# Kernel tuning notes

Measured on AMD Instinct MI355X. Metric: run time of the kernel, lower is better.

## Reference

```python
import jax, jax.numpy as jnp
import numpy as np

K = 9            # kernel_size * dilation
ALPHA = 0.2      # LeakyReLU slope in GAT attention
LRELU = 0.01     # Grapher.layer1 default LeakyReLU slope
EPS_NORM = 1e-12
BN_EPS = 1e-5
NEG_INF = -9e15


def setup_inputs() -> dict:
    key = jax.random.key(0)
    ks = jax.random.split(key, 9)
    B, C, H, W = 16, 64, 32, 32
    nheads, nhid = 4, 15
    return {
        "x": jax.random.normal(ks[0], (B, C, H, W), jnp.float32),
        "W_heads": jax.random.normal(ks[1], (nheads, C, nhid), jnp.float32) * 0.2,
        "a_heads": jax.random.normal(ks[2], (nheads, 2 * nhid, 1), jnp.float32) * 0.2,
        "W_out": jax.random.normal(ks[3], (nheads * nhid, C), jnp.float32) * 0.2,
        "a_out": jax.random.normal(ks[4], (2 * C, 1), jnp.float32) * 0.2,
        "conv_w": jax.random.normal(ks[5], (C, C), jnp.float32) * 0.1,
        "conv_b": jax.random.normal(ks[6], (C,), jnp.float32) * 0.1,
        "bn_gamma": jnp.ones((C,), jnp.float32),
        "bn_beta": jnp.zeros((C,), jnp.float32),
    }


def _gat_layer(h, adj, W, a, concat):
    # h: [B,N,Fin], W: [Fin,Fout], a: [2*Fout,1]
    Wh = h @ W                                   # [B,N,Fout]
    Fout = W.shape[1]
    f1 = Wh @ a[:Fout]                           # [B,N,1]  (a . Wh_i)
    f2 = Wh @ a[Fout:]                           # [B,N,1]  (a . Wh_j)
    e = jax.nn.leaky_relu(f1 + jnp.swapaxes(f2, 1, 2), ALPHA)  # [B,N,N]
    att = jnp.where(adj > 0, e, NEG_INF)
    att = jax.nn.softmax(att, axis=1)            # torch F.softmax(dim=1)
    hp = att @ Wh                                # [B,N,Fout]
    return jax.nn.elu(hp) if concat else hp


def reference(x, W_heads, a_heads, W_out, a_out, conv_w, conv_b, bn_gamma, bn_beta):
    B, C, H, W = x.shape
    N = H * W
    res = x
    xf = x.reshape(B, C, N)                      # [B,C,N]
    # F.normalize(p=2, dim=1)
    nrm = jnp.maximum(jnp.linalg.norm(xf, axis=1, keepdims=True), EPS_NORM)
    h = jnp.swapaxes(xf / nrm, 1, 2)             # [B,N,C]
    # KNN adjacency (built under no_grad in the original)
    hs = jax.lax.stop_gradient(h)
    sq = jnp.sum(hs * hs, axis=-1, keepdims=True)        # [B,N,1]
    dist = sq - 2.0 * (hs @ jnp.swapaxes(hs, 1, 2)) + jnp.swapaxes(sq, 1, 2)
    _, idx = jax.lax.top_k(-dist, K)                      # [B,N,K]
    adj = jnp.zeros((B, N, N), x.dtype).at[
        jnp.arange(B)[:, None, None], jnp.arange(N)[None, :, None], idx
    ].set(1.0)
    # 4-head GAT (dropout is identity in eval mode)
    heads = [_gat_layer(h, adj, W_heads[i], a_heads[i], True)
             for i in range(W_heads.shape[0])]
    hcat = jnp.concatenate(heads, axis=2)        # [B,N,60]
    out = jax.nn.elu(_gat_layer(hcat, adj, W_out, a_out, False))  # [B,N,C]
    y = jnp.swapaxes(out, 1, 2).reshape(B, C, H, W)
    y = jax.nn.leaky_relu(y, LRELU)
    # 1x1 conv + BatchNorm (eval: running_mean=0, running_var=1)
    y = jnp.einsum('bchw,oc->bohw', y, conv_w) + conv_b[None, :, None, None]
    y = y / jnp.sqrt(1.0 + BN_EPS) * bn_gamma[None, :, None, None] + bn_beta[None, :, None, None]
    return y + res
```

## Files before the change

kernel.cpp:

```cpp
#include <hip/hip_runtime.h>
#include <math.h>

#define NB 16
#define NC 64
#define NN 1024
#define NK 9
#define NH 4
#define NF 15

#define OFF_HN     0
#define OFF_SQV    1048576
#define OFF_IDX    1064960
#define OFF_DEN1   1212416
#define OFF_U1     1277952
#define OFF_DEN2   1278976
#define OFF_U2     1295360
#define OFF_F11    1296384
#define OFF_F21    1361920
#define OFF_F12    1427456
#define OFF_F22    1443840
#define OFF_E1     1460224
#define OFF_E2     2050048
#define OFF_WH1    2197504
#define OFF_HCAT   3246080
#define OFF_WH2    4294656
#define OFF_YTIL   5343232
#define OFF_DIST   6391808
#define ZERO_BASE  OFF_DEN1
#define ZERO_LEN   83968

__device__ __forceinline__ unsigned fkey(float x){
  unsigned b = __float_as_uint(x);
  return (b & 0x80000000u) ? ~b : (b | 0x80000000u);
}
__device__ __forceinline__ float eluf(float x){ return x > 0.f ? x : expm1f(x); }

__global__ __launch_bounds__(256) void k1_norm_wh(const float* __restrict__ x,
    const float* __restrict__ W_heads, const float* __restrict__ a_heads,
    float* __restrict__ hn, float* __restrict__ sqv, float* __restrict__ Wh1,
    float* __restrict__ f1, float* __restrict__ f2, float* __restrict__ ws){
  int t = blockIdx.x*256 + threadIdx.x;
  if (t < ZERO_LEN) ws[ZERO_BASE + t] = 0.f;
  if (t >= NB*NN) return;
  int b = t >> 10, n = t & 1023;
  const float* xb = x + b*NC*NN;
  float* hb = hn + b*NC*NN;
  float s = 0.f;
  #pragma unroll
  for (int c = 0; c < NC; c++){ float v = xb[c*NN + n]; s = fmaf(v, v, s); }
  float nrm = fmaxf(sqrtf(s), 1e-12f);
  float wh[NH][NF];
  #pragma unroll
  for (int hh = 0; hh < NH; hh++)
    #pragma unroll
    for (int f = 0; f < NF; f++) wh[hh][f] = 0.f;
  float s2 = 0.f;
  for (int c = 0; c < NC; c++){
    float v = xb[c*NN + n] / nrm;
    hb[c*NN + n] = v;
    s2 = fmaf(v, v, s2);
    #pragma unroll
    for (int hh = 0; hh < NH; hh++){
      const float* W = W_heads + (hh*NC + c)*NF;
      #pragma unroll
      for (int f = 0; f < NF; f++) wh[hh][f] = fmaf(v, W[f], wh[hh][f]);
    }
  }
  sqv[t] = s2;
  float* orow = Wh1 + ((size_t)(b*NN) + n)*64;
  #pragma unroll
  for (int hh = 0; hh < NH; hh++){
    const float* al = a_heads + hh*2*NF;
    float s1 = 0.f, sb = 0.f;
    #pragma unroll
    for (int f = 0; f < NF; f++){ s1 = fmaf(wh[hh][f], al[f], s1); sb = fmaf(wh[hh][f], al[NF+f], sb); }
    float4* o4 = (float4*)(orow + hh*16);
    o4[0] = make_float4(wh[hh][0], wh[hh][1], wh[hh][2], wh[hh][3]);
    o4[1] = make_float4(wh[hh][4], wh[hh][5], wh[hh][6], wh[hh][7]);
    o4[2] = make_float4(wh[hh][8], wh[hh][9], wh[hh][10], wh[hh][11]);
    o4[3] = make_float4(wh[hh][12], wh[hh][13], wh[hh][14], 0.f);
    int hb2 = hh*NB + b;
    f1[hb2*NN + n] = s1; f2[hb2*NN + n] = sb;
  }
}

__global__ __launch_bounds__(256) void k2a_dist(const float* __restrict__ hn,
    const float* __restrict__ sqv, float* __restrict__ dist){
  __shared__ float As[64][128];
  __shared__ float Bs[64][128];
  int b = blockIdx.y;
  int i0 = (blockIdx.x >> 3) * 128, j0 = (blockIdx.x & 7) * 128;
  const float* hb = hn + b*NC*NN;
  for (int t = threadIdx.x; t < 64*128; t += 256){
    int c = t >> 7, ii = t & 127;
    As[c][ii] = hb[c*NN + i0 + ii];
    Bs[c][ii] = hb[c*NN + j0 + ii];
  }
  __syncthreads();
  int tx = threadIdx.x & 15, ty = threadIdx.x >> 4;
  float acc[8][8];
  #pragma unroll
  for (int q = 0; q < 8; q++)
    #pragma unroll
    for (int jj = 0; jj < 8; jj++) acc[q][jj] = 0.f;
  #pragma unroll 4
  for (int c = 0; c < 64; c++){
    float4 a0 = *(const float4*)&As[c][ty*8];
    float4 a1 = *(const float4*)&As[c][ty*8+4];
    float4 b0 = *(const float4*)&Bs[c][tx*8];
    float4 b1 = *(const float4*)&Bs[c][tx*8+4];
    float av[8], bv[8];
    av[0]=a0.x; av[1]=a0.y; av[2]=a0.z; av[3]=a0.w; av[4]=a1.x; av[5]=a1.y; av[6]=a1.z; av[7]=a1.w;
    bv[0]=b0.x; bv[1]=b0.y; bv[2]=b0.z; bv[3]=b0.w; bv[4]=b1.x; bv[5]=b1.y; bv[6]=b1.z; bv[7]=b1.w;
    #pragma unroll
    for (int q = 0; q < 8; q++)
      #pragma unroll
      for (int jj = 0; jj < 8; jj++) acc[q][jj] = fmaf(av[q], bv[jj], acc[q][jj]);
  }
  const float* sv = sqv + b*NN;
  float sj[8];
  #pragma unroll
  for (int jj = 0; jj < 8; jj++) sj[jj] = sv[j0 + tx*8 + jj];
  #pragma unroll
  for (int q = 0; q < 8; q++){
    float si = sv[i0 + ty*8 + q];
    float o0[8];
    #pragma unroll
    for (int jj = 0; jj < 8; jj++) o0[jj] = (si - 2.f*acc[q][jj]) + sj[jj];
    float* dp = dist + (size_t)((b*NN) + i0 + ty*8 + q)*NN + j0 + tx*8;
    *(float4*)&dp[0] = make_float4(o0[0],o0[1],o0[2],o0[3]);
    *(float4*)&dp[4] = make_float4(o0[4],o0[5],o0[6],o0[7]);
  }
}

__global__ __launch_bounds__(256) void k2b_top9e(const float* __restrict__ dist,
    int* __restrict__ idxb, const float* __restrict__ f1, const float* __restrict__ f2,
    float* __restrict__ e1, float* __restrict__ den1){
  __shared__ int sj[4][16];
  int wave = threadIdx.x >> 6, lane = threadIdx.x & 63;
  int t = blockIdx.x*4 + wave;
  int b = t >> 10, i = t & 1023;
  const float* dr = dist + (size_t)t*NN;
  unsigned long long key[16];
  #pragma unroll
  for (int m = 0; m < 16; m++){
    int j = m*64 + lane;
    key[m] = ((unsigned long long)fkey(dr[j]) << 32) | (unsigned)j;
  }
  for (int round = 0; round < NK; round++){
    unsigned long long best = key[0];
    #pragma unroll
    for (int m = 1; m < 16; m++) best = key[m] < best ? key[m] : best;
    #pragma unroll
    for (int off = 32; off >= 1; off >>= 1){
      unsigned long long o = __shfl_xor(best, off);
      best = o < best ? o : best;
    }
    if (lane == 0) sj[wave][round] = (int)(best & 0xFFFFFFFFu);
    int wl = (int)(best & 63u);
    int wm = (int)((best >> 6) & 15u);
    if (lane == wl) key[wm] = ~0ull;
  }
  __syncthreads();
  if (lane < NK) idxb[(size_t)t*NK + lane] = sj[wave][lane];
  if (lane < 36){
    int k = lane >> 2, hh = lane & 3;
    int j = sj[wave][k];
    int hb = hh*NB + b;
    float e = f1[hb*NN + i] + f2[hb*NN + j];
    e = e >= 0.f ? e : 0.2f*e;
    e1[(size_t)(hb*NN + i)*NK + k] = e;
    atomicAdd(den1 + hb*NN + j, expf(e));
  }
}

__global__ __launch_bounds__(256) void k4b_u1(const float* __restrict__ denom1,
                       const float* __restrict__ Wh1, float* __restrict__ u1){
  int t = blockIdx.x*256 + threadIdx.x;
  if (denom1[t] != 0.f) return;
  int hb = t >> 10, j = t & 1023;
  int hh = hb >> 4, b = hb & 15;
  const float* w = Wh1 + ((size_t)(b*NN) + j)*64 + hh*16;
  for (int f = 0; f < NF; f++) atomicAdd(u1 + hb*16 + f, w[f] * (1.f/1024.f));
}

__global__ __launch_bounds__(256) void k5_hp1(const int* __restrict__ idxb, const float* __restrict__ e1,
    const float* __restrict__ denom1, const float* __restrict__ Wh1,
    const float* __restrict__ u1, float* __restrict__ hcat){
  int wave = threadIdx.x >> 6, lane = threadIdx.x & 63;
  int t = blockIdx.x*4 + wave;
  int b = t >> 10, i = t & 1023;
  int hh = lane >> 4, f = lane & 15;
  int hb = hh*NB + b;
  float acc = u1[hb*16 + f];
  const int* jp = idxb + (size_t)t*NK;
  const float* ep = e1 + (size_t)(hb*NN + i)*NK;
  const float* dn = denom1 + hb*NN;
  const float* wbase = Wh1 + ((size_t)(b*NN))*64;
  #pragma unroll 3
  for (int k = 0; k < NK; k++){
    int j = jp[k];
    float att = expf(ep[k]) / dn[j];
    acc = fmaf(att, wbase[(size_t)j*64 + lane], acc);
  }
  if (f < NF) hcat[((size_t)(b*NN) + i)*64 + hh*NF + f] = eluf(acc);
}

__global__ __launch_bounds__(256) void k7_wh2(const float* __restrict__ hcat,
    const float* __restrict__ W_out, const float* __restrict__ a_out,
    float* __restrict__ Wh2, float* __restrict__ f1, float* __restrict__ f2){
  __shared__ float hcl[64][65];
  __shared__ float p1[4][64], p2[4][64];
  int b = blockIdx.y, n0 = blockIdx.x*64;
  for (int t = threadIdx.x; t < 4096; t += 256){
    int nl = t >> 6, c = t & 63;
    hcl[nl][c] = hcat[(size_t)((b*NN) + n0 + nl)*64 + c];
  }
  __syncthreads();
  int nl = threadIdx.x & 63;
  int wv = threadIdx.x >> 6;
  int og = __builtin_amdgcn_readfirstlane(wv * 16);
  float z[16];
  #pragma unroll
  for (int m = 0; m < 16; m++) z[m] = 0.f;
  for (int c = 0; c < 60; c++){
    float yv = hcl[nl][c];
    #pragma unroll
    for (int m = 0; m < 16; m++) z[m] = fmaf(yv, W_out[c*64 + og + m], z[m]);
  }
  int n = n0 + nl;
  float* o = Wh2 + ((size_t)(b*NN) + n)*64 + og;
  #pragma unroll
  for (int m = 0; m < 16; m += 4) *(float4*)&o[m] = make_float4(z[m],z[m+1],z[m+2],z[m+3]);
  float s1 = 0.f, s2 = 0.f;
  #pragma unroll
  for (int m = 0; m < 16; m++){ s1 = fmaf(z[m], a_out[og+m], s1); s2 = fmaf(z[m], a_out[64+og+m], s2); }
  p1[wv][nl] = s1; p2[wv][nl] = s2;
  __syncthreads();
  if (threadIdx.x < 64){
    f1[b*NN + n0 + threadIdx.x] = p1[0][threadIdx.x] + p1[1][threadIdx.x] + p1[2][threadIdx.x] + p1[3][threadIdx.x];
    f2[b*NN + n0 + threadIdx.x] = p2[0][threadIdx.x] + p2[1][threadIdx.x] + p2[2][threadIdx.x] + p2[3][threadIdx.x];
  }
}

__global__ __launch_bounds__(256) void k8_edge2(const int* __restrict__ idxb, const float* __restrict__ f1,
                         const float* __restrict__ f2, float* __restrict__ e2,
                         float* __restrict__ denom2){
  int t = blockIdx.x*256 + threadIdx.x;
  int bi = t / 9;
  int b = bi >> 10;
  int j = idxb[t];
  float e = f1[bi] + f2[b*NN + j];
  e = e >= 0.f ? e : 0.2f*e;
  e2[t] = e;
  atomicAdd(denom2 + b*NN + j, expf(e));
}

__global__ __launch_bounds__(256) void k8b_u2(const float* __restrict__ denom2,
                       const float* __restrict__ Wh2, float* __restrict__ u2){
  int t = blockIdx.x*256 + threadIdx.x;
  if (denom2[t] != 0.f) return;
  int b = t >> 10;
  const float* w = Wh2 + (size_t)t*64;
  for (int f = 0; f < 64; f++) atomicAdd(u2 + b*64 + f, w[f] * (1.f/1024.f));
}

__global__ __launch_bounds__(256) void k9_hp2(const int* __restrict__ idxb, const float* __restrict__ e2,
    const float* __restrict__ denom2, const float* __restrict__ Wh2,
    const float* __restrict__ u2, float* __restrict__ ytil){
  int wave = threadIdx.x >> 6, lane = threadIdx.x & 63;
  int t = blockIdx.x*4 + wave;
  int b = t >> 10;
  float acc = u2[b*64 + lane];
  const int* jp = idxb + (size_t)t*NK;
  const float* ep = e2 + (size_t)t*NK;
  const float* dn = denom2 + b*NN;
  const float* wbase = Wh2 + ((size_t)(b*NN))*64;
  #pragma unroll 3
  for (int k = 0; k < NK; k++){
    int j = jp[k];
    float att = expf(ep[k]) / dn[j];
    acc = fmaf(att, wbase[(size_t)j*64 + lane], acc);
  }
  float v = eluf(acc);
  ytil[(size_t)t*64 + lane] = v >= 0.f ? v : 0.01f*v;
}

__global__ __launch_bounds__(256) void k11_conv(const float* __restrict__ ytil,
    const float* __restrict__ conv_w, const float* __restrict__ conv_b,
    const float* __restrict__ bn_g, const float* __restrict__ bn_b,
    const float* __restrict__ x, float* __restrict__ out){
  __shared__ float yt[64][65];
  int b = blockIdx.y, n0 = blockIdx.x*64;
  for (int t = threadIdx.x; t < 4096; t += 256){
    int nl = t >> 6, c = t & 63;
    yt[nl][c] = ytil[(size_t)((b*NN) + n0 + nl)*64 + c];
  }
  __syncthreads();
  int nl = threadIdx.x & 63;
  int og = __builtin_amdgcn_readfirstlane((int)(threadIdx.x >> 6) * 16);
  float z[16];
  #pragma unroll
  for (int m = 0; m < 16; m++) z[m] = 0.f;
  for (int c = 0; c < 64; c++){
    float yv = yt[nl][c];
    #pragma unroll
    for (int m = 0; m < 16; m++) z[m] = fmaf(yv, conv_w[(og+m)*64 + c], z[m]);
  }
  const float scbn = 1.f / sqrtf(1.f + 1e-5f);
  #pragma unroll
  for (int m = 0; m < 16; m++){
    int o = og + m;
    size_t oi = ((size_t)(b*64 + o))*NN + n0 + nl;
    out[oi] = fmaf(z[m] + conv_b[o], bn_g[o]*scbn, bn_b[o]) + x[oi];
  }
}

extern "C" void kernel_launch(void* const* d_in, const int* in_sizes, int n_in,
                              void* d_out, int out_size, void* d_ws, size_t ws_size,
                              hipStream_t stream){
  (void)in_sizes; (void)n_in; (void)out_size; (void)ws_size;
  const float* x       = (const float*)d_in[0];
  const float* W_heads = (const float*)d_in[1];
  const float* a_heads = (const float*)d_in[2];
  const float* W_out   = (const float*)d_in[3];
  const float* a_out   = (const float*)d_in[4];
  const float* conv_w  = (const float*)d_in[5];
  const float* conv_b  = (const float*)d_in[6];
  const float* bn_g    = (const float*)d_in[7];
  const float* bn_b    = (const float*)d_in[8];
  float* ws  = (float*)d_ws;
  float* out = (float*)d_out;

  float* hn   = ws + OFF_HN;
  float* sqv  = ws + OFF_SQV;
  int*   idxb = (int*)(ws + OFF_IDX);
  float* den1 = ws + OFF_DEN1;
  float* u1   = ws + OFF_U1;
  float* den2 = ws + OFF_DEN2;
  float* u2   = ws + OFF_U2;
  float* f11  = ws + OFF_F11;
  float* f21  = ws + OFF_F21;
  float* f12  = ws + OFF_F12;
  float* f22  = ws + OFF_F22;
  float* e1   = ws + OFF_E1;
  float* e2   = ws + OFF_E2;
  float* Wh1  = ws + OFF_WH1;
  float* hcat = ws + OFF_HCAT;
  float* Wh2  = ws + OFF_WH2;
  float* ytil = ws + OFF_YTIL;
  float* dist = ws + OFF_DIST;

  k1_norm_wh<<<dim3(328), dim3(256), 0, stream>>>(x, W_heads, a_heads, hn, sqv, Wh1, f11, f21, ws);
  k2a_dist<<<dim3(64,16), dim3(256), 0, stream>>>(hn, sqv, dist);
  k2b_top9e<<<dim3(4096), dim3(256), 0, stream>>>(dist, idxb, f11, f21, e1, den1);
  k4b_u1<<<dim3(256), dim3(256), 0, stream>>>(den1, Wh1, u1);
  k5_hp1<<<dim3(4096), dim3(256), 0, stream>>>(idxb, e1, den1, Wh1, u1, hcat);
  k7_wh2<<<dim3(16,16), dim3(256), 0, stream>>>(hcat, W_out, a_out, Wh2, f12, f22);
  k8_edge2<<<dim3(576), dim3(256), 0, stream>>>(idxb, f12, f22, e2, den2);
  k8b_u2<<<dim3(64), dim3(256), 0, stream>>>(den2, Wh2, u2);
  k9_hp2<<<dim3(4096), dim3(256), 0, stream>>>(idxb, e2, den2, Wh2, u2, ytil);
  k11_conv<<<dim3(16,16), dim3(256), 0, stream>>>(ytil, conv_w, conv_b, bn_g, bn_b, x, out);
}
```

Baseline: 270.3 us.

## Fuse KNN distance GEMM with per-row top-9 selection and edge scoring

Replaces the separate distance-matrix kernel and top-k kernel with one kernel that tiles the Gram product over 64-column tiles in shared memory and keeps a per-thread sorted 9-entry candidate list, then merges four partial lists per row with shuffles. This removes writing and re-reading the full B×N×N distance buffer in global memory and one launch. In exchange only 256 blocks run, each thread holds many 64-bit registers for the candidate list, and the insertion step is serial and branchy, which may limit occupancy and parallelism.

```diff
diff --git a/kernel.cpp b/kernel.cpp
--- a/kernel.cpp
+++ b/kernel.cpp
@@ -25,7 +25,6 @@
 #define OFF_HCAT   3246080
 #define OFF_WH2    4294656
 #define OFF_YTIL   5343232
-#define OFF_DIST   6391808
 #define ZERO_BASE  OFF_DEN1
 #define ZERO_LEN   83968
 
@@ -84,93 +83,107 @@
   }
 }
 
-__global__ __launch_bounds__(256) void k2a_dist(const float* __restrict__ hn,
-    const float* __restrict__ sqv, float* __restrict__ dist){
-  __shared__ float As[64][128];
-  __shared__ float Bs[64][128];
-  int b = blockIdx.y;
-  int i0 = (blockIdx.x >> 3) * 128, j0 = (blockIdx.x & 7) * 128;
+#define LSTR 68
+__global__ __launch_bounds__(256) void k2_knn(const float* __restrict__ hn,
+    const float* __restrict__ sqv, const float* __restrict__ f1g, const float* __restrict__ f2g,
+    int* __restrict__ idxb, float* __restrict__ e1, float* __restrict__ den1){
+  __shared__ float As[64][LSTR];
+  __shared__ float Bs[64][LSTR];
+  __shared__ float Ds[64][LSTR];
+  __shared__ float ssq[64], sjq[64];
+  int b  = blockIdx.y;
+  int i0 = blockIdx.x * 64;
+  int tid = threadIdx.x;
   const float* hb = hn + b*NC*NN;
-  for (int t = threadIdx.x; t < 64*128; t += 256){
-    int c = t >> 7, ii = t & 127;
-    As[c][ii] = hb[c*NN + i0 + ii];
-    Bs[c][ii] = hb[c*NN + j0 + ii];
-  }
-  __syncthreads();
-  int tx = threadIdx.x & 15, ty = threadIdx.x >> 4;
-  float acc[8][8];
-  #pragma unroll
-  for (int q = 0; q < 8; q++)
-    #pragma unroll
-    for (int jj = 0; jj < 8; jj++) acc[q][jj] = 0.f;
-  #pragma unroll 4
-  for (int c = 0; c < 64; c++){
-    float4 a0 = *(const float4*)&As[c][ty*8];
-    float4 a1 = *(const float4*)&As[c][ty*8+4];
-    float4 b0 = *(const float4*)&Bs[c][tx*8];
-    float4 b1 = *(const float4*)&Bs[c][tx*8+4];
-    float av[8], bv[8];
-    av[0]=a0.x; av[1]=a0.y; av[2]=a0.z; av[3]=a0.w; av[4]=a1.x; av[5]=a1.y; av[6]=a1.z; av[7]=a1.w;
-    bv[0]=b0.x; bv[1]=b0.y; bv[2]=b0.z; bv[3]=b0.w; bv[4]=b1.x; bv[5]=b1.y; bv[6]=b1.z; bv[7]=b1.w;
-    #pragma unroll
-    for (int q = 0; q < 8; q++)
+  #pragma unroll
+  for (int k = 0; k < 4; k++){
+    int idx4 = tid + k*256;
+    int c = idx4 >> 4, q4 = (idx4 & 15) * 4;
+    *(float4*)&As[c][q4] = *(const float4*)&hb[c*NN + i0 + q4];
+  }
+  if (tid < 64) ssq[tid] = sqv[b*NN + i0 + tid];
+  int rg = tid >> 4, cg = tid & 15;
+  int r  = tid >> 2, p  = tid & 3;
+  unsigned long long s0=~0ull,s1=~0ull,s2k=~0ull,s3=~0ull,s4=~0ull,s5=~0ull,s6=~0ull,s7=~0ull,s8=~0ull;
+  for (int jt = 0; jt < 16; jt++){
+    int j0 = jt * 64;
+    __syncthreads();
+    #pragma unroll
+    for (int k = 0; k < 4; k++){
+      int idx4 = tid + k*256;
+      int c = idx4 >> 4, q4 = (idx4 & 15) * 4;
+      *(float4*)&Bs[c][q4] = *(const float4*)&hb[c*NN + j0 + q4];
+    }
+    if (tid < 64) sjq[tid] = sqv[b*NN + j0 + tid];
+    __syncthreads();
+    float acc[4][4];
+    #pragma unroll
+    for (int q = 0; q < 4; q++)
       #pragma unroll
-      for (int jj = 0; jj < 8; jj++) acc[q][jj] = fmaf(av[q], bv[jj], acc[q][jj]);
-  }
-  const float* sv = sqv + b*NN;
-  float sj[8];
-  #pragma unroll
-  for (int jj = 0; jj < 8; jj++) sj[jj] = sv[j0 + tx*8 + jj];
-  #pragma unroll
-  for (int q = 0; q < 8; q++){
-    float si = sv[i0 + ty*8 + q];
-    float o0[8];
-    #pragma unroll
-    for (int jj = 0; jj < 8; jj++) o0[jj] = (si - 2.f*acc[q][jj]) + sj[jj];
-    float* dp = dist + (size_t)((b*NN) + i0 + ty*8 + q)*NN + j0 + tx*8;
-    *(float4*)&dp[0] = make_float4(o0[0],o0[1],o0[2],o0[3]);
-    *(float4*)&dp[4] = make_float4(o0[4],o0[5],o0[6],o0[7]);
-  }
-}
-
-__global__ __launch_bounds__(256) void k2b_top9e(const float* __restrict__ dist,
-    int* __restrict__ idxb, const float* __restrict__ f1, const float* __restrict__ f2,
-    float* __restrict__ e1, float* __restrict__ den1){
-  __shared__ int sj[4][16];
-  int wave = threadIdx.x >> 6, lane = threadIdx.x & 63;
-  int t = blockIdx.x*4 + wave;
-  int b = t >> 10, i = t & 1023;
-  const float* dr = dist + (size_t)t*NN;
-  unsigned long long key[16];
-  #pragma unroll
-  for (int m = 0; m < 16; m++){
-    int j = m*64 + lane;
-    key[m] = ((unsigned long long)fkey(dr[j]) << 32) | (unsigned)j;
-  }
+      for (int jj = 0; jj < 4; jj++) acc[q][jj] = 0.f;
+    #pragma unroll 4
+    for (int c = 0; c < 64; c++){
+      float4 a  = *(const float4*)&As[c][rg*4];
+      float4 bb = *(const float4*)&Bs[c][cg*4];
+      float av[4] = {a.x, a.y, a.z, a.w};
+      float bv[4] = {bb.x, bb.y, bb.z, bb.w};
+      #pragma unroll
+      for (int q = 0; q < 4; q++)
+        #pragma unroll
+        for (int jj = 0; jj < 4; jj++) acc[q][jj] = fmaf(av[q], bv[jj], acc[q][jj]);
+    }
+    #pragma unroll
+    for (int q = 0; q < 4; q++){
+      float si = ssq[rg*4+q];
+      float4 o;
+      o.x = (si - 2.f*acc[q][0]) + sjq[cg*4+0];
+      o.y = (si - 2.f*acc[q][1]) + sjq[cg*4+1];
+      o.z = (si - 2.f*acc[q][2]) + sjq[cg*4+2];
+      o.w = (si - 2.f*acc[q][3]) + sjq[cg*4+3];
+      *(float4*)&Ds[rg*4+q][cg*4] = o;
+    }
+    __syncthreads();
+    #pragma unroll
+    for (int m = 0; m < 4; m++){
+      float4 v = *(const float4*)&Ds[r][p*16 + m*4];
+      float vv[4] = {v.x, v.y, v.z, v.w};
+      #pragma unroll
+      for (int q = 0; q < 4; q++){
+        unsigned long long kk = ((unsigned long long)fkey(vv[q]) << 32)
+                              | (unsigned)(j0 + p*16 + m*4 + q);
+        if (kk < s8){
+          s8 = kk;
+          unsigned long long tt;
+          if (s8 < s7){ tt=s7; s7=s8; s8=tt; }
+          if (s7 < s6){ tt=s6; s6=s7; s7=tt; }
+          if (s6 < s5){ tt=s5; s5=s6; s6=tt; }
+          if (s5 < s4){ tt=s4; s4=s5; s5=tt; }
+          if (s4 < s3){ tt=s3; s3=s4; s4=tt; }
+          if (s3 < s2k){ tt=s2k; s2k=s3; s3=tt; }
+          if (s2k < s1){ tt=s1; s1=s2k; s2k=tt; }
+          if (s1 < s0){ tt=s0; s0=s1; s1=tt; }
+        }
+      }
+    }
+  }
+  int i = i0 + r;
+  int hbh = p*NB + b;
+  float f1v = f1g[hbh*NN + i];
+  unsigned long long h = s0;
+  #pragma unroll
   for (int round = 0; round < NK; round++){
-    unsigned long long best = key[0];
-    #pragma unroll
-    for (int m = 1; m < 16; m++) best = key[m] < best ? key[m] : best;
-    #pragma unroll
-    for (int off = 32; off >= 1; off >>= 1){
-      unsigned long long o = __shfl_xor(best, off);
-      best = o < best ? o : best;
-    }
-    if (lane == 0) sj[wave][round] = (int)(best & 0xFFFFFFFFu);
-    int wl = (int)(best & 63u);
-    int wm = (int)((best >> 6) & 15u);
-    if (lane == wl) key[wm] = ~0ull;
-  }
-  __syncthreads();
-  if (lane < NK) idxb[(size_t)t*NK + lane] = sj[wave][lane];
-  if (lane < 36){
-    int k = lane >> 2, hh = lane & 3;
-    int j = sj[wave][k];
-    int hb = hh*NB + b;
-    float e = f1[hb*NN + i] + f2[hb*NN + j];
+    unsigned long long g = h;
+    unsigned long long o1 = __shfl_xor(g, 1); g = o1 < g ? o1 : g;
+    unsigned long long o2 = __shfl_xor(g, 2); g = o2 < g ? o2 : g;
+    if (h == g){
+      s0=s1; s1=s2k; s2k=s3; s3=s4; s4=s5; s5=s6; s6=s7; s7=s8; s8=~0ull; h=s0;
+    }
+    int j = (int)(g & 0xFFFFFFFFu);
+    if (p == 0) idxb[((size_t)(b*NN) + i)*NK + round] = j;
+    float e = f1v + f2g[hbh*NN + j];
     e = e >= 0.f ? e : 0.2f*e;
-    e1[(size_t)(hb*NN + i)*NK + k] = e;
-    atomicAdd(den1 + hb*NN + j, expf(e));
+    e1[((size_t)(hbh*NN) + i)*NK + round] = e;
+    atomicAdd(den1 + hbh*NN + j, expf(e));
   }
 }
 
@@ -349,11 +362,9 @@
   float* hcat = ws + OFF_HCAT;
   float* Wh2  = ws + OFF_WH2;
   float* ytil = ws + OFF_YTIL;
-  float* dist = ws + OFF_DIST;
 
   k1_norm_wh<<<dim3(328), dim3(256), 0, stream>>>(x, W_heads, a_heads, hn, sqv, Wh1, f11, f21, ws);
-  k2a_dist<<<dim3(64,16), dim3(256), 0, stream>>>(hn, sqv, dist);
-  k2b_top9e<<<dim3(4096), dim3(256), 0, stream>>>(dist, idxb, f11, f21, e1, den1);
+  k2_knn<<<dim3(16,16), dim3(256), 0, stream>>>(hn, sqv, f11, f21, idxb, e1, den1);
   k4b_u1<<<dim3(256), dim3(256), 0, stream>>>(den1, Wh1, u1);
   k5_hp1<<<dim3(4096), dim3(256), 0, stream>>>(idxb, e1, den1, Wh1, u1, hcat);
   k7_wh2<<<dim3(16,16), dim3(256), 0, stream>>>(hcat, W_out, a_out, Wh2, f12, f22);
```

Measured after the change: 284.4 us. 1.05x slower.
